# Kernel optimization log

Measured on AMD Instinct MI355X. Metric: run time of the kernel, lower is better.

The kernel has to match this reference:

```python
import jax, jax.numpy as jnp
import numpy as np

N = 50000
E = 1_600_000
F_IN = 128
HID = 64
OUT = 2
NEG_SLOPE = 0.2  # PyG GATConv default


def setup_inputs() -> dict:
    key = jax.random.key(0)
    ks = jax.random.split(key, 10)
    x = jax.random.normal(ks[0], (N, F_IN), jnp.float32)
    edge_index = jax.random.randint(ks[1], (2, E), 0, N, dtype=jnp.int32)
    # glorot-ish scaled params
    W1 = jax.random.normal(ks[2], (F_IN, HID), jnp.float32) / np.sqrt(F_IN)
    a1_src = jax.random.normal(ks[3], (HID,), jnp.float32) / np.sqrt(HID)
    a1_dst = jax.random.normal(ks[4], (HID,), jnp.float32) / np.sqrt(HID)
    b1 = jnp.zeros((HID,), jnp.float32)
    W2 = jax.random.normal(ks[5], (HID, OUT), jnp.float32) / np.sqrt(HID)
    a2_src = jax.random.normal(ks[6], (OUT,), jnp.float32) / np.sqrt(OUT)
    a2_dst = jax.random.normal(ks[7], (OUT,), jnp.float32) / np.sqrt(OUT)
    b2 = jnp.zeros((OUT,), jnp.float32)
    return {"x": x, "edge_index": edge_index, "W1": W1, "a1_src": a1_src,
            "a1_dst": a1_dst, "b1": b1, "W2": W2, "a2_src": a2_src,
            "a2_dst": a2_dst, "b2": b2}


def gat_layer(x, edge_index, W, a_src, a_dst, b):
    n = x.shape[0]
    loop = jnp.arange(n, dtype=edge_index.dtype)
    src = jnp.concatenate([edge_index[0], loop])  # [E+N] message sources j
    dst = jnp.concatenate([edge_index[1], loop])  # [E+N] message targets i
    h = x @ W                                     # [N, out]
    alpha_s = h @ a_src                           # [N]
    alpha_d = h @ a_dst                           # [N]
    e = jax.nn.leaky_relu(alpha_s[src] + alpha_d[dst], NEG_SLOPE)  # [E+N]
    # segment softmax over edges sharing the same destination node
    emax = jax.ops.segment_max(e, dst, num_segments=n)
    ee = jnp.exp(e - emax[dst])
    denom = jax.ops.segment_sum(ee, dst, num_segments=n)
    alpha = ee / denom[dst]
    out = jax.ops.segment_sum(alpha[:, None] * h[src], dst, num_segments=n)
    return out + b


def reference(x, edge_index, W1, a1_src, a1_dst, b1, W2, a2_src, a2_dst, b2):
    h = gat_layer(x, edge_index, W1, a1_src, a1_dst, b1)
    h = jax.nn.relu(h)
    # dropout(p=0.5) is identity in eval mode
    return gat_layer(h, edge_index, W2, a2_src, a2_dst, b2)
```

## Files before the change

### kernel.cpp

```cpp
#include <hip/hip_runtime.h>
#include <math.h>


#define NEG 0.2f
#define NEGINF (-1e30f)

#define BPW   128
#define NB    391
#define BLKS  192
#define SCAP  64
#define CAPB  4864

__device__ __forceinline__ float leaky(float v) { return v >= 0.f ? v : NEG * v; }

__global__ __launch_bounds__(256) void k_gemm_bucket(
    const float* __restrict__ x, const float* __restrict__ W1,
    const float* __restrict__ a1s_, const float* __restrict__ a1d_,
    const int* __restrict__ esrc, const int* __restrict__ edst, int N, int E,
    float* __restrict__ h1, float* __restrict__ as1, float* __restrict__ ad1,
    int* __restrict__ slabs, int* __restrict__ slabcnt) {
    __shared__ float xs[16 * 128];
    __shared__ int cnt[NB];
    int nbG = (N + 15) / 16;
    int t = threadIdx.x;
    if ((int)blockIdx.x < nbG) {
        {
            const float4* xg = (const float4*)x;
            float4* xs4 = (float4*)xs;
            int nf4 = N * 32;
            int g0 = blockIdx.x * 512 + t;
            int g1 = g0 + 256;
            xs4[t]       = (g0 < nf4) ? xg[g0] : make_float4(0.f, 0.f, 0.f, 0.f);
            xs4[t + 256] = (g1 < nf4) ? xg[g1] : make_float4(0.f, 0.f, 0.f, 0.f);
        }
        __syncthreads();
        int lane = t & 63, wid = t >> 6;
        int r0 = blockIdx.x * 16 + wid * 4;
        if (r0 >= N) return;
        const float4* x0 = (const float4*)(xs + (wid * 4 + 0) * 128);
        const float4* x1 = (const float4*)(xs + (wid * 4 + 1) * 128);
        const float4* x2 = (const float4*)(xs + (wid * 4 + 2) * 128);
        const float4* x3 = (const float4*)(xs + (wid * 4 + 3) * 128);
        float acc0 = 0.f, acc1 = 0.f, acc2 = 0.f, acc3 = 0.f;
#pragma unroll 8
        for (int k4 = 0; k4 < 32; k4++) {
            int kb = k4 * 4;
            float w0 = W1[(kb + 0) * 64 + lane];
            float w1 = W1[(kb + 1) * 64 + lane];
            float w2 = W1[(kb + 2) * 64 + lane];
            float w3 = W1[(kb + 3) * 64 + lane];
            float4 a = x0[k4], bb = x1[k4], c = x2[k4], d = x3[k4];
            acc0 = fmaf(a.x, w0, fmaf(a.y, w1, fmaf(a.z, w2, fmaf(a.w, w3, acc0))));
            acc1 = fmaf(bb.x, w0, fmaf(bb.y, w1, fmaf(bb.z, w2, fmaf(bb.w, w3, acc1))));
            acc2 = fmaf(c.x, w0, fmaf(c.y, w1, fmaf(c.z, w2, fmaf(c.w, w3, acc2))));
            acc3 = fmaf(d.x, w0, fmaf(d.y, w1, fmaf(d.z, w2, fmaf(d.w, w3, acc3))));
        }
        float asv = a1s_[lane], adv = a1d_[lane];
        float accs[4] = {acc0, acc1, acc2, acc3};
#pragma unroll
        for (int r = 0; r < 4; r++) {
            int row = r0 + r;
            if (row < N) h1[(size_t)row * 64 + lane] = accs[r];
            float ts = accs[r] * asv, td = accs[r] * adv;
            for (int m = 32; m > 0; m >>= 1) {
                ts += __shfl_xor(ts, m, 64);
                td += __shfl_xor(td, m, 64);
            }
            if (lane == 0 && row < N) { as1[row] = ts; ad1[row] = td; }
        }
    } else {
        int blk = blockIdx.x - nbG;
        for (int i = t; i < NB; i += 256) cnt[i] = 0;
        __syncthreads();
        int chunk = (E + BLKS - 1) / BLKS;
        int lo = blk * chunk, hi = min(E, lo + chunk);
        for (int e = lo + t; e < hi; e += 256) {
            int s = esrc[e], d = edst[e];
            int b = d >> 7;
            int pos = atomicAdd(&cnt[b], 1);
            if (pos < SCAP)
                slabs[(b * BLKS + blk) * SCAP + pos] = s | ((d & 127) << 16);
        }
        __syncthreads();
        for (int i = t; i < NB; i += 256)
            slabcnt[blk * NB + i] = min(cnt[i], SCAP);
    }
}

__global__ __launch_bounds__(256) void k_sortb(
    const int* __restrict__ slabs, const int* __restrict__ slabcnt, int N,
    int* __restrict__ ssrc32, int* __restrict__ nodebase,
    int* __restrict__ nodedeg) {
    __shared__ int stage[BLKS * SCAP];
    __shared__ unsigned short outs[CAPB];
    __shared__ int ccnt[BLKS];
    __shared__ int hist[BPW], pexcl[BPW], cur[BPW];
    __shared__ int btotS;
    int b = blockIdx.x, t = threadIdx.x;

    for (int i = t; i < BLKS; i += 256) ccnt[i] = slabcnt[i * NB + b];
    for (int i = t; i < BPW; i += 256) hist[i] = 0;
    __syncthreads();

    const int4* src4 = (const int4*)(slabs + (size_t)b * BLKS * SCAP);
    int4* st4 = (int4*)stage;
    for (int i = t; i < (BLKS * SCAP) / 4; i += 256) st4[i] = src4[i];
    __syncthreads();

    for (int i = t; i < BLKS * SCAP; i += 256) {
        int cell = i >> 6, pos = i & (SCAP - 1);
        if (pos < ccnt[cell]) atomicAdd(&hist[stage[i] >> 16], 1);
    }
    __syncthreads();

    if (t < 64) {
        int h0 = hist[2 * t], h1v = hist[2 * t + 1];
        int p0 = (h0 + 3) & ~3, p1 = (h1v + 3) & ~3;
        int ps = p0 + p1, incl = ps;
        for (int off = 1; off < 64; off <<= 1) {
            int u = __shfl_up(incl, off, 64);
            if (t >= off) incl += u;
        }
        int ex = incl - ps;
        pexcl[2 * t] = ex;          cur[2 * t] = ex;
        pexcl[2 * t + 1] = ex + p0; cur[2 * t + 1] = ex + p0;
        if (t == 63) btotS = incl;
    }
    __syncthreads();

    for (int i = t; i < BLKS * SCAP; i += 256) {
        int cell = i >> 6, pos = i & (SCAP - 1);
        if (pos < ccnt[cell]) {
            int en = stage[i];
            int p = atomicAdd(&cur[en >> 16], 1);
            if (p < CAPB) outs[p] = (unsigned short)(en & 0xFFFF);
        }
    }
    __syncthreads();

    int v0 = b * BPW;
    for (int i = t; i < BPW; i += 256) {
        int h = hist[i], ph = (h + 3) & ~3;
        for (int j = h; j < ph; j++) {
            int pos = pexcl[i] + j;
            if (pos < CAPB) outs[pos] = (unsigned short)(v0 + i);
        }
    }
    __syncthreads();

    int btot = min(btotS, CAPB);
    int* dst = ssrc32 + (size_t)b * CAPB;
    for (int i = t; i < btot; i += 256) dst[i] = (int)outs[i];

    for (int i = t; i < BPW; i += 256) {
        int v = v0 + i;
        if (v < N) { nodebase[v] = b * CAPB + pexcl[i]; nodedeg[v] = hist[i]; }
    }
}

__global__ __launch_bounds__(256) void k_agg1f(
    const float* __restrict__ h1, const float* __restrict__ as1,
    const float* __restrict__ ad1, const int* __restrict__ nodebase,
    const int* __restrict__ nodedeg, const int* __restrict__ ssrc32,
    const float* __restrict__ b1, const float* __restrict__ W2,
    const float* __restrict__ a2s, const float* __restrict__ a2d, int N,
    float4* __restrict__ node4) {
    __shared__ __align__(16) float pw[4][128];
    int lane = threadIdx.x & 63;
    int wid = __builtin_amdgcn_readfirstlane(threadIdx.x >> 6);
    int i = blockIdx.x * 4 + wid;
    if (i >= N) return;
    float ad_i = ad1[i];
    int base = nodebase[i], deg = nodedeg[i];

    float e0 = NEGINF, e1 = NEGINF;
    if (lane < deg)      e0 = leaky(as1[ssrc32[base + lane]] + ad_i);
    if (lane + 64 < deg) e1 = leaky(as1[ssrc32[base + lane + 64]] + ad_i);
    float ml = fmaxf(e0, e1), sl = 0.f;
    for (int t = base + lane + 128; t < base + deg; t += 64) {
        float e = leaky(as1[ssrc32[t]] + ad_i);
        float mN = fmaxf(ml, e);
        sl = sl * __expf(ml - mN) + __expf(e - mN);
        ml = mN;
    }
    sl += __expf(e0 - ml) + __expf(e1 - ml);
    for (int off = 32; off > 0; off >>= 1) {
        float m2 = __shfl_xor(ml, off, 64);
        float s2 = __shfl_xor(sl, off, 64);
        float mN = fmaxf(ml, m2);
        sl = sl * __expf(ml - mN) + s2 * __expf(m2 - mN);
        ml = mN;
    }
    float e_self = leaky(as1[i] + ad_i);
    float m = fmaxf(ml, e_self);
    float s = sl * __expf(ml - m) + __expf(e_self - m);
    float inv_s = 1.f / s;

    pw[wid][lane]      = (lane < deg)      ? __expf(e0 - m) * inv_s : 0.f;
    pw[wid][lane + 64] = (lane + 64 < deg) ? __expf(e1 - m) * inv_s : 0.f;

    int nq = (min(deg, 128) + 3) >> 2;
    const int4* sq = (const int4*)(ssrc32 + base);
    float acc = __expf(e_self - m) * inv_s * h1[(size_t)i * 64 + lane];
#pragma unroll 2
    for (int q = 0; q < nq; ++q) {
        int4 s4 = sq[q];
        float4 p4 = *(const float4*)&pw[wid][q * 4];
        float g0 = h1[(size_t)s4.x * 64 + lane];
        float g1 = h1[(size_t)s4.y * 64 + lane];
        float g2 = h1[(size_t)s4.z * 64 + lane];
        float g3 = h1[(size_t)s4.w * 64 + lane];
        acc = fmaf(p4.x, g0, acc);
        acc = fmaf(p4.y, g1, acc);
        acc = fmaf(p4.z, g2, acc);
        acc = fmaf(p4.w, g3, acc);
    }
    for (int t = base + 128; t < base + deg; ++t) {
        int sv = ssrc32[t];
        float p = __expf(leaky(as1[sv] + ad_i) - m) * inv_s;
        acc = fmaf(p, h1[(size_t)sv * 64 + lane], acc);
    }

    float hr = fmaxf(acc + b1[lane], 0.f);
    float2 w2 = ((const float2*)W2)[lane];
    float t0 = hr * w2.x, t1 = hr * w2.y;
    for (int mm = 32; mm > 0; mm >>= 1) {
        t0 += __shfl_xor(t0, mm, 64);
        t1 += __shfl_xor(t1, mm, 64);
    }
    if (lane == 0) {
        float s0 = t0 * a2s[0] + t1 * a2s[1];
        float d0 = t0 * a2d[0] + t1 * a2d[1];
        node4[i] = make_float4(t0, t1, s0, d0);
    }
}

__global__ __launch_bounds__(256) void k_agg2(
    const float4* __restrict__ node4, const int* __restrict__ nodebase,
    const int* __restrict__ nodedeg, const int* __restrict__ ssrc32,
    const float* __restrict__ b2, int N, float2* __restrict__ out) {
    int lane = threadIdx.x & 63, wid = threadIdx.x >> 6;
    int i = blockIdx.x * 4 + wid;
    if (i >= N) return;
    float4 ni = node4[i];
    float adi = ni.w;
    int base = nodebase[i], end = base + nodedeg[i];
    float ml = NEGINF, sl = 0.f, A0 = 0.f, A1 = 0.f;
    for (int t = base + lane; t < end; t += 64) {
        float4 nd = node4[ssrc32[t]];
        float e = leaky(nd.z + adi);
        float mN = fmaxf(ml, e);
        float c1 = __expf(ml - mN), p = __expf(e - mN);
        sl = fmaf(sl, c1, p);
        A0 = fmaf(A0, c1, p * nd.x);
        A1 = fmaf(A1, c1, p * nd.y);
        ml = mN;
    }
    for (int off = 32; off > 0; off >>= 1) {
        float m2 = __shfl_xor(ml, off, 64);
        float s2 = __shfl_xor(sl, off, 64);
        float a02 = __shfl_xor(A0, off, 64);
        float a12 = __shfl_xor(A1, off, 64);
        float mN = fmaxf(ml, m2);
        float c1 = __expf(ml - mN), c2 = __expf(m2 - mN);
        sl = sl * c1 + s2 * c2;
        A0 = A0 * c1 + a02 * c2;
        A1 = A1 * c1 + a12 * c2;
        ml = mN;
    }
    float e_self = leaky(ni.z + adi);
    float mN = fmaxf(ml, e_self);
    float c1 = __expf(ml - mN), c2 = __expf(e_self - mN);
    float s = sl * c1 + c2;
    float a0 = A0 * c1 + c2 * ni.x;
    float a1 = A1 * c1 + c2 * ni.y;
    if (lane == 0) out[i] = make_float2(a0 / s + b2[0], a1 / s + b2[1]);
}

extern "C" void kernel_launch(void* const* d_in, const int* in_sizes, int n_in,
                              void* d_out, int out_size, void* d_ws, size_t ws_size,
                              hipStream_t stream) {
    const float* x   = (const float*)d_in[0];
    const int*   ei  = (const int*)d_in[1];
    const float* W1  = (const float*)d_in[2];
    const float* a1s = (const float*)d_in[3];
    const float* a1d = (const float*)d_in[4];
    const float* b1  = (const float*)d_in[5];
    const float* W2  = (const float*)d_in[6];
    const float* a2s = (const float*)d_in[7];
    const float* a2d = (const float*)d_in[8];
    const float* b2  = (const float*)d_in[9];

    int N = in_sizes[0] / 128;
    int E = in_sizes[1] / 2;
    const int* esrc = ei;
    const int* edst = ei + E;

    float*  h1    = (float*)d_ws;
    float*  as1   = h1 + (size_t)N * 64;
    float*  ad1   = as1 + N;
    float*  pad0  = ad1 + N;
    float4* node4 = (float4*)(pad0 + N);
    int* slabs    = (int*)(node4 + N);
    int* slabcnt  = slabs + (size_t)NB * BLKS * SCAP;
    int* ssrc32   = slabcnt + (size_t)BLKS * NB;
    int* nodebase = ssrc32 + (size_t)NB * CAPB;
    int* nodedeg  = nodebase + N;

    int nbG = (N + 15) / 16;
    k_gemm_bucket<<<nbG + BLKS, 256, 0, stream>>>(x, W1, a1s, a1d, esrc, edst,
                                                  N, E, h1, as1, ad1, slabs, slabcnt);
    k_sortb<<<NB, 256, 0, stream>>>(slabs, slabcnt, N, ssrc32, nodebase, nodedeg);
    k_agg1f<<<(N + 3) / 4, 256, 0, stream>>>(h1, as1, ad1, nodebase, nodedeg,
                                             ssrc32, b1, W2, a2s, a2d, N, node4);
    k_agg2<<<(N + 3) / 4, 256, 0, stream>>>(node4, nodebase, nodedeg, ssrc32, b2,
                                            N, (float2*)d_out);
}
```

Baseline: 222.8 us.

## Use more bucketing blocks with smaller slabs and compact slab staging in sort

Raises the number of edge-bucketing blocks to 768 and halves the per-cell slab capacity. The bucketing blocks are moved ahead of the GEMM blocks in the fused launch so the scatter work starts first. The sort kernel now prefix-sums the cell counts and copies only the valid entries into a compact shared stage, where before it loaded the full fixed-size slab array and masked it. This is meant to spread the bucketing over more CUs and reduce shared-memory footprint and wasted work in the sort. The per-thread compaction loop reads cells serially and uncoalesced, and the smaller slabs raise the risk of overflow truncation (about 5.3 edges expected per cell).

```diff
diff --git a/kernel.cpp b/kernel.cpp
--- a/kernel.cpp
+++ b/kernel.cpp
@@ -7,8 +7,8 @@
 
 #define BPW   128
 #define NB    391
-#define BLKS  192
-#define SCAP  64
+#define BLKS  768
+#define SCAP  32
 #define CAPB  4864
 
 __device__ __forceinline__ float leaky(float v) { return v >= 0.f ? v : NEG * v; }
@@ -21,21 +21,37 @@
     int* __restrict__ slabs, int* __restrict__ slabcnt) {
     __shared__ float xs[16 * 128];
     __shared__ int cnt[NB];
-    int nbG = (N + 15) / 16;
     int t = threadIdx.x;
-    if ((int)blockIdx.x < nbG) {
+    if ((int)blockIdx.x < BLKS) {
+        int blk = blockIdx.x;
+        for (int i = t; i < NB; i += 256) cnt[i] = 0;
+        __syncthreads();
+        int chunk = (E + BLKS - 1) / BLKS;
+        int lo = blk * chunk, hi = min(E, lo + chunk);
+        for (int e = lo + t; e < hi; e += 256) {
+            int s = esrc[e], d = edst[e];
+            int b = d >> 7;
+            int pos = atomicAdd(&cnt[b], 1);
+            if (pos < SCAP)
+                slabs[((size_t)b * BLKS + blk) * SCAP + pos] = s | ((d & 127) << 16);
+        }
+        __syncthreads();
+        for (int i = t; i < NB; i += 256)
+            slabcnt[i * BLKS + blk] = min(cnt[i], SCAP);
+    } else {
+        int gb = blockIdx.x - BLKS;
         {
             const float4* xg = (const float4*)x;
             float4* xs4 = (float4*)xs;
             int nf4 = N * 32;
-            int g0 = blockIdx.x * 512 + t;
+            int g0 = gb * 512 + t;
             int g1 = g0 + 256;
             xs4[t]       = (g0 < nf4) ? xg[g0] : make_float4(0.f, 0.f, 0.f, 0.f);
             xs4[t + 256] = (g1 < nf4) ? xg[g1] : make_float4(0.f, 0.f, 0.f, 0.f);
         }
         __syncthreads();
         int lane = t & 63, wid = t >> 6;
-        int r0 = blockIdx.x * 16 + wid * 4;
+        int r0 = gb * 16 + wid * 4;
         if (r0 >= N) return;
         const float4* x0 = (const float4*)(xs + (wid * 4 + 0) * 128);
         const float4* x1 = (const float4*)(xs + (wid * 4 + 1) * 128);
@@ -68,22 +84,6 @@
             }
             if (lane == 0 && row < N) { as1[row] = ts; ad1[row] = td; }
         }
-    } else {
-        int blk = blockIdx.x - nbG;
-        for (int i = t; i < NB; i += 256) cnt[i] = 0;
-        __syncthreads();
-        int chunk = (E + BLKS - 1) / BLKS;
-        int lo = blk * chunk, hi = min(E, lo + chunk);
-        for (int e = lo + t; e < hi; e += 256) {
-            int s = esrc[e], d = edst[e];
-            int b = d >> 7;
-            int pos = atomicAdd(&cnt[b], 1);
-            if (pos < SCAP)
-                slabs[(b * BLKS + blk) * SCAP + pos] = s | ((d & 127) << 16);
-        }
-        __syncthreads();
-        for (int i = t; i < NB; i += 256)
-            slabcnt[blk * NB + i] = min(cnt[i], SCAP);
     }
 }
 
@@ -91,26 +91,46 @@
     const int* __restrict__ slabs, const int* __restrict__ slabcnt, int N,
     int* __restrict__ ssrc32, int* __restrict__ nodebase,
     int* __restrict__ nodedeg) {
-    __shared__ int stage[BLKS * SCAP];
+    __shared__ int cstage[CAPB];
     __shared__ unsigned short outs[CAPB];
     __shared__ int ccnt[BLKS];
+    __shared__ int coff[BLKS];
     __shared__ int hist[BPW], pexcl[BPW], cur[BPW];
-    __shared__ int btotS;
+    __shared__ int ctotS, btotS;
     int b = blockIdx.x, t = threadIdx.x;
 
-    for (int i = t; i < BLKS; i += 256) ccnt[i] = slabcnt[i * NB + b];
+    for (int i = t; i < BLKS; i += 256) ccnt[i] = slabcnt[b * BLKS + i];
     for (int i = t; i < BPW; i += 256) hist[i] = 0;
     __syncthreads();
 
-    const int4* src4 = (const int4*)(slabs + (size_t)b * BLKS * SCAP);
-    int4* st4 = (int4*)stage;
-    for (int i = t; i < (BLKS * SCAP) / 4; i += 256) st4[i] = src4[i];
-    __syncthreads();
-
-    for (int i = t; i < BLKS * SCAP; i += 256) {
-        int cell = i >> 6, pos = i & (SCAP - 1);
-        if (pos < ccnt[cell]) atomicAdd(&hist[stage[i] >> 16], 1);
-    }
+    if (t < 64) {
+        int carry = 0;
+        for (int c0 = 0; c0 < BLKS; c0 += 64) {
+            int v = ccnt[c0 + t];
+            int incl = v;
+            for (int off = 1; off < 64; off <<= 1) {
+                int u = __shfl_up(incl, off, 64);
+                if (t >= off) incl += u;
+            }
+            coff[c0 + t] = carry + incl - v;
+            carry += __shfl(incl, 63, 64);
+        }
+        if (t == 0) ctotS = carry;
+    }
+    __syncthreads();
+    int ctot = min(ctotS, CAPB);
+
+    for (int c = t; c < BLKS; c += 256) {
+        int cn = ccnt[c], off = coff[c];
+        const int* cell = slabs + ((size_t)b * BLKS + c) * SCAP;
+        for (int j = 0; j < cn; j++) {
+            int p = off + j;
+            if (p < CAPB) cstage[p] = cell[j];
+        }
+    }
+    __syncthreads();
+
+    for (int i = t; i < ctot; i += 256) atomicAdd(&hist[cstage[i] >> 16], 1);
     __syncthreads();
 
     if (t < 64) {
@@ -128,13 +148,10 @@
     }
     __syncthreads();
 
-    for (int i = t; i < BLKS * SCAP; i += 256) {
-        int cell = i >> 6, pos = i & (SCAP - 1);
-        if (pos < ccnt[cell]) {
-            int en = stage[i];
-            int p = atomicAdd(&cur[en >> 16], 1);
-            if (p < CAPB) outs[p] = (unsigned short)(en & 0xFFFF);
-        }
+    for (int i = t; i < ctot; i += 256) {
+        int en = cstage[i];
+        int p = atomicAdd(&cur[en >> 16], 1);
+        if (p < CAPB) outs[p] = (unsigned short)(en & 0xFFFF);
     }
     __syncthreads();
 
@@ -303,12 +320,12 @@
     float4* node4 = (float4*)(pad0 + N);
     int* slabs    = (int*)(node4 + N);
     int* slabcnt  = slabs + (size_t)NB * BLKS * SCAP;
-    int* ssrc32   = slabcnt + (size_t)BLKS * NB;
+    int* ssrc32   = slabcnt + (size_t)NB * BLKS;
     int* nodebase = ssrc32 + (size_t)NB * CAPB;
     int* nodedeg  = nodebase + N;
 
     int nbG = (N + 15) / 16;
-    k_gemm_bucket<<<nbG + BLKS, 256, 0, stream>>>(x, W1, a1s, a1d, esrc, edst,
+    k_gemm_bucket<<<BLKS + nbG, 256, 0, stream>>>(x, W1, a1s, a1d, esrc, edst,
                                                   N, E, h1, as1, ad1, slabs, slabcnt);
     k_sortb<<<NB, 256, 0, stream>>>(slabs, slabcnt, N, ssrc32, nodebase, nodedeg);
     k_agg1f<<<(N + 3) / 4, 256, 0, stream>>>(h1, as1, ad1, nodebase, nodedeg,
```

Result: faster. 217.5 us (-2.4%).
